# Kernel optimization log

Measured on AMD Instinct MI355X. Metric: run time of the kernel, lower is better.

The kernel has to match this reference:

```python
import jax, jax.numpy as jnp
import numpy as np

FACTOR = 0.2          # rotation/zoom/shift factor (init kwarg)
SCALE = 1.0 / 255.0   # rescale (init kwarg)
TWO_PI = 6.283185307179586
B, H, W, C = 64, 224, 224, 3


def _reflect(i, n):
    # TF fill_mode='reflect' index mapping (symmetric with edge repeat)
    m = jnp.mod(i, 2 * n)
    return jnp.where(m >= n, 2 * n - 1 - m, m)


def _bilinear(img, xs, ys):
    # img [H,W,C]; xs, ys [H,W] = input-space sample coords for each output pixel
    h, w, _ = img.shape
    x0f = jnp.floor(xs)
    y0f = jnp.floor(ys)
    fx = (xs - x0f)[..., None]
    fy = (ys - y0f)[..., None]
    x0 = x0f.astype(jnp.int32)
    y0 = y0f.astype(jnp.int32)
    x0r = _reflect(x0, w); x1r = _reflect(x0 + 1, w)
    y0r = _reflect(y0, h); y1r = _reflect(y0 + 1, h)
    Ia = img[y0r, x0r]; Ib = img[y0r, x1r]
    Ic = img[y1r, x0r]; Id = img[y1r, x1r]
    top = Ia * (1.0 - fx) + Ib * fx
    bot = Ic * (1.0 - fx) + Id * fx
    return top * (1.0 - fy) + bot * fy


_warp = jax.vmap(_bilinear)  # over batch: images [B,H,W,C], coords [B,H,W]


def setup_inputs() -> dict:
    key = jax.random.key(0)
    k = jax.random.split(key, 5)
    return {
        "image": jax.random.uniform(k[0], (B, H, W, C), jnp.float32) * 255.0,
        "angle_u": jax.random.uniform(k[1], (B,), jnp.float32),
        "zoom_u": jax.random.uniform(k[2], (B, 2), jnp.float32),
        "shift_u": jax.random.uniform(k[3], (B, 2), jnp.float32),
        "flip_u": jax.random.uniform(k[4], (B,), jnp.float32),
    }


def reference(image, angle_u, zoom_u, shift_u, flip_u):
    b, h, w, _ = image.shape
    dt = image.dtype
    yy, xx = jnp.meshgrid(jnp.arange(h, dtype=dt), jnp.arange(w, dtype=dt), indexing='ij')
    cx = (w - 1) / 2.0
    cy = (h - 1) / 2.0

    # 1) rescale
    x = image * SCALE

    # 2) random rotation: angle uniform in [-factor*2pi, +factor*2pi]
    theta = (2.0 * angle_u - 1.0) * FACTOR * TWO_PI            # [B]
    c = jnp.cos(theta)[:, None, None]
    s = jnp.sin(theta)[:, None, None]
    xr = c * (xx - cx) - s * (yy - cy) + cx                    # [B,H,W]
    yr = s * (xx - cx) + c * (yy - cy) + cy
    x = _warp(x, xr, yr)

    # 3) random zoom: zoom factor uniform in [1-factor, 1+factor] per axis
    z = 1.0 + (2.0 * zoom_u - 1.0) * FACTOR                    # [B,2] (h, w)
    zh = z[:, 0][:, None, None]
    zw = z[:, 1][:, None, None]
    xz = zw * (xx - cx) + cx
    yz = zh * (yy - cy) + cy
    x = _warp(x, xz, yz)

    # 4) random translation: shift fraction uniform in [-factor, factor]
    sh = (2.0 * shift_u - 1.0) * FACTOR                        # [B,2] (h, w)
    dy = (sh[:, 0] * h)[:, None, None]
    dx = (sh[:, 1] * w)[:, None, None]
    xt = xx - dx
    yt = yy - dy
    x = _warp(x, xt, yt)

    # 5) random horizontal flip (p = 0.5)
    flip = flip_u > 0.5
    x = jnp.where(flip[:, None, None, None], x[:, :, ::-1, :], x)
    return x
```

## Files before the change

kernel.cpp:

```cpp
#include <hip/hip_runtime.h>
#include <hip/hip_fp16.h>
#include <math.h>

#define BB 64
#define HH 224
#define WW 224
#define CC 3

constexpr float FACTOR  = 0.2f;
constexpr float SCALE_K = 1.0f / 255.0f;
constexpr float TWO_PI_F = 6.283185307179586f;
constexpr float CX = (WW - 1) * 0.5f;
constexpr float CY = (HH - 1) * 0.5f;
constexpr int PIX = HH * WW;
constexpr int IMG_ELEMS = PIX * CC;

constexpr int TILES_X = WW / 16;
constexpr int TILES_PER_IMG = TILES_X * TILES_X;
constexpr int NXCD = 8;
constexpr int NBLOCKS = BB * TILES_PER_IMG;

typedef float f32x4 __attribute__((ext_vector_type(4), aligned(4)));
typedef unsigned int u32x4 __attribute__((ext_vector_type(4), aligned(8)));

__device__ __forceinline__ int reflect1(int i, int n) {
    i = (i < 0) ? (-1 - i) : i;
    return (i >= n) ? (2 * n - 1 - i) : i;
}

__device__ __forceinline__ void rhull(int a, int b, int n, int& lo, int& hi) {
    int ra = reflect1(a, n), rb = reflect1(b, n);
    lo = min(ra, rb); hi = max(ra, rb);
    if (a <= 0 && b >= -1) lo = 0;
    if (b >= n - 1 && a <= n) hi = n - 1;
}

__device__ __forceinline__ void decode_tile(int bid, int& b, int& tx, int& ty) {
    int xcd  = bid & (NXCD - 1);
    int slot = bid >> 3;
    int bi   = slot / TILES_PER_IMG;
    int t    = slot - bi * TILES_PER_IMG;
    b = xcd + bi * NXCD;
    ty = t / TILES_X;
    tx = t - ty * TILES_X;
}

__device__ __forceinline__ void up3(uint2 v, float* o) {
    o[0] = __half2float(__ushort_as_half((unsigned short)(v.x & 0xffffu)));
    o[1] = __half2float(__ushort_as_half((unsigned short)(v.x >> 16)));
    o[2] = __half2float(__ushort_as_half((unsigned short)(v.y & 0xffffu)));
}

__device__ __forceinline__ uint2 pack3(float a, float b, float c) {
    uint2 v;
    v.x = (unsigned)__half_as_ushort(__float2half_rn(a)) |
          ((unsigned)__half_as_ushort(__float2half_rn(b)) << 16);
    v.y = (unsigned)__half_as_ushort(__float2half_rn(c));
    return v;
}

__global__ __launch_bounds__(256)
void rotate_kernel(const float* __restrict__ image, uint2* __restrict__ tmp,
                   const float* __restrict__ angle_u) {
    __shared__ float4 S[24][33];
    int b, tx, ty;
    decode_tile(blockIdx.x, b, tx, ty);
    const int ox = tx * 16, oy = ty * 16;

    const float theta = (2.0f * angle_u[b] - 1.0f) * FACTOR * TWO_PI_F;
    const float c = __cosf(theta), s = __sinf(theta);

    const float rx0 = (float)ox - CX, rx1 = (float)(ox + 15) - CX;
    const float ry0 = (float)oy - CY, ry1 = (float)(oy + 15) - CY;
    const int Xlo = (int)floorf(fminf(c * rx0, c * rx1) + fminf(-s * ry0, -s * ry1) + CX);
    const int Xhi = (int)floorf(fmaxf(c * rx0, c * rx1) + fmaxf(-s * ry0, -s * ry1) + CX) + 1;
    const int Ylo = (int)floorf(fminf(s * rx0, s * rx1) + fminf(c * ry0, c * ry1) + CY);
    const int Yhi = (int)floorf(fmaxf(s * rx0, s * rx1) + fmaxf(c * ry0, c * ry1) + CY) + 1;
    int Cx0, Cx1, Cy0, Cy1;
    rhull(Xlo, Xhi, WW, Cx0, Cx1);
    rhull(Ylo, Yhi, HH, Cy0, Cy1);

    const float* img = image + (size_t)b * IMG_ELEMS;
    {
        const int lc  = threadIdx.x & 31;
        const int col = min(Cx0 + lc, WW - 1);
#pragma unroll
        for (int it = 0; it < 3; ++it) {
            const int r   = it * 8 + (threadIdx.x >> 5);
            const int row = min(Cy0 + r, HH - 1);
            int pe = (row * WW + col) * CC;
            const bool last = pe > IMG_ELEMS - 4;
            pe = min(pe, IMG_ELEMS - 4);
            f32x4 v = *(const f32x4*)(img + pe);
            S[r][lc] = last ? make_float4(v.y, v.z, v.w, 0.0f)
                            : make_float4(v.x, v.y, v.z, v.w);
        }
    }
    __syncthreads();

    const int x = ox + (threadIdx.x & 15), y = oy + (threadIdx.x >> 4);
    const float xs = c * ((float)x - CX) - s * ((float)y - CY) + CX;
    const float ys = s * ((float)x - CX) + c * ((float)y - CY) + CY;
    const float xf = floorf(xs), yf = floorf(ys);
    const float fx = xs - xf, fy = ys - yf;
    const int x0 = (int)xf, y0 = (int)yf;
    const int c0 = min(max(reflect1(x0,     WW) - Cx0, 0), 31);
    const int c1 = min(max(reflect1(x0 + 1, WW) - Cx0, 0), 31);
    const int r0 = min(max(reflect1(y0,     HH) - Cy0, 0), 23);
    const int r1 = min(max(reflect1(y0 + 1, HH) - Cy0, 0), 23);

    const float4 A  = S[r0][c0];
    const float4 Bv = S[r0][c1];
    const float4 Cv = S[r1][c0];
    const float4 Dv = S[r1][c1];

    const float ofx = 1.0f - fx, ofy = 1.0f - fy;
    const float o0 = ((A.x * ofx + Bv.x * fx) * ofy + (Cv.x * ofx + Dv.x * fx) * fy) * SCALE_K;
    const float o1 = ((A.y * ofx + Bv.y * fx) * ofy + (Cv.y * ofx + Dv.y * fx) * fy) * SCALE_K;
    const float o2 = ((A.z * ofx + Bv.z * fx) * ofy + (Cv.z * ofx + Dv.z * fx) * fy) * SCALE_K;

    tmp[(size_t)b * PIX + y * WW + x] = pack3(o0, o1, o2);
}

__global__ __launch_bounds__(256)
void zoomshift_kernel(const uint2* __restrict__ tmp, float* __restrict__ out,
                      const float* __restrict__ zoom_u,
                      const float* __restrict__ shift_u,
                      const float* __restrict__ flip_u) {
    __shared__ uint2 Sz[32][34];
    __shared__ uint2 Zl[17][18];
    int b, tx, ty;
    decode_tile(blockIdx.x, b, tx, ty);
    const int ox = tx * 16, oy = ty * 16;

    const float zh = 1.0f + (2.0f * zoom_u[2 * b + 0] - 1.0f) * FACTOR;
    const float zw = 1.0f + (2.0f * zoom_u[2 * b + 1] - 1.0f) * FACTOR;
    const float dy = ((2.0f * shift_u[2 * b + 0] - 1.0f) * FACTOR) * (float)HH;
    const float dx = ((2.0f * shift_u[2 * b + 1] - 1.0f) * FACTOR) * (float)WW;
    const bool flip = flip_u[b] > 0.5f;

    const float ndxf = floorf(-dx), ndyf = floorf(-dy);
    const int Kx = (int)ndxf, Ky = (int)ndyf;
    const float fx3 = -dx - ndxf, fy3 = -dy - ndyf;

    const int Xmin = (flip ? WW - 16 - ox : ox) + Kx;
    const int Ymin = oy + Ky;

    int XrLo, XrHi, YrLo, YrHi;
    rhull(Xmin, Xmin + 16, WW, XrLo, XrHi);
    rhull(Ymin, Ymin + 16, HH, YrLo, YrHi);

    const int Gx0 = (int)floorf(zw * ((float)XrLo - CX) + CX);
    const int Gx1 = (int)floorf(zw * ((float)XrHi - CX) + CX) + 1;
    const int Gy0 = (int)floorf(zh * ((float)YrLo - CY) + CY);
    const int Gy1 = (int)floorf(zh * ((float)YrHi - CY) + CY) + 1;
    int Cx0, Cx1, Cy0, Cy1;
    rhull(Gx0, Gx1, WW, Cx0, Cx1);
    rhull(Gy0, Gy1, HH, Cy0, Cy1);
    const int CxA = Cx0 & ~1;

    const uint2* timg = tmp + (size_t)b * PIX;
    {
        const int cp  = (threadIdx.x & 15) * 2;
        const int col = min(CxA + cp, WW - 2);
#pragma unroll
        for (int it = 0; it < 2; ++it) {
            const int r   = it * 16 + (threadIdx.x >> 4);
            const int row = min(Cy0 + r, HH - 1);
            u32x4 v = *(const u32x4*)(timg + row * WW + col);
            *(u32x4*)(&Sz[r][cp]) = v;
        }
    }
    __syncthreads();

    for (int e = threadIdx.x; e < 17 * 17; e += 256) {
        const int ey = e / 17, ex = e - ey * 17;
        const int Xr = reflect1(Xmin + ex, WW);
        const int Yr = reflect1(Ymin + ey, HH);
        const float xs2 = zw * ((float)Xr - CX) + CX;
        const float ys2 = zh * ((float)Yr - CY) + CY;
        const float xf = floorf(xs2), yf = floorf(ys2);
        const float fx2 = xs2 - xf, fy2 = ys2 - yf;
        const int x20 = (int)xf, y20 = (int)yf;
        const int cA = min(max(reflect1(x20,     WW) - CxA, 0), 31);
        const int cB = min(max(reflect1(x20 + 1, WW) - CxA, 0), 31);
        const int rA = min(max(reflect1(y20,     HH) - Cy0, 0), 31);
        const int rB = min(max(reflect1(y20 + 1, HH) - Cy0, 0), 31);

        float A[3], Bv[3], Cv[3], Dv[3];
        up3(Sz[rA][cA], A);  up3(Sz[rA][cB], Bv);
        up3(Sz[rB][cA], Cv); up3(Sz[rB][cB], Dv);

        const float ofx = 1.0f - fx2, ofy = 1.0f - fy2;
        const float z0 = (A[0] * ofx + Bv[0] * fx2) * ofy + (Cv[0] * ofx + Dv[0] * fx2) * fy2;
        const float z1 = (A[1] * ofx + Bv[1] * fx2) * ofy + (Cv[1] * ofx + Dv[1] * fx2) * fy2;
        const float z2 = (A[2] * ofx + Bv[2] * fx2) * ofy + (Cv[2] * ofx + Dv[2] * fx2) * fy2;
        Zl[ey][ex] = pack3(z0, z1, z2);
    }
    __syncthreads();

    const int lx = threadIdx.x & 15, ly = threadIdx.x >> 4;
    const int ix = flip ? (15 - lx) : lx;
    float A[3], Bv[3], Cv[3], Dv[3];
    up3(Zl[ly][ix],     A);  up3(Zl[ly][ix + 1],     Bv);
    up3(Zl[ly + 1][ix], Cv); up3(Zl[ly + 1][ix + 1], Dv);

    float* o = out + ((size_t)b * PIX + (size_t)(oy + ly) * WW + (ox + lx)) * CC;
    const float ofx = 1.0f - fx3, ofy = 1.0f - fy3;
    o[0] = (A[0] * ofx + Bv[0] * fx3) * ofy + (Cv[0] * ofx + Dv[0] * fx3) * fy3;
    o[1] = (A[1] * ofx + Bv[1] * fx3) * ofy + (Cv[1] * ofx + Dv[1] * fx3) * fy3;
    o[2] = (A[2] * ofx + Bv[2] * fx3) * ofy + (Cv[2] * ofx + Dv[2] * fx3) * fy3;
}

extern "C" void kernel_launch(void* const* d_in, const int* in_sizes, int n_in,
                              void* d_out, int out_size, void* d_ws, size_t ws_size,
                              hipStream_t stream) {
    const float* image   = (const float*)d_in[0];
    const float* angle_u = (const float*)d_in[1];
    const float* zoom_u  = (const float*)d_in[2];
    const float* shift_u = (const float*)d_in[3];
    const float* flip_u  = (const float*)d_in[4];
    float* out = (float*)d_out;

    uint2* tmp = (uint2*)d_ws;

    rotate_kernel<<<NBLOCKS, 256, 0, stream>>>(image, tmp, angle_u);
    zoomshift_kernel<<<NBLOCKS, 256, 0, stream>>>(tmp, out, zoom_u, shift_u, flip_u);
}
```

Baseline: 42.03 us.

## Fuse rotate and zoom/shift warps into a single kernel with recompute halo

Merges the two-kernel pipeline into one kernel. Each output tile back-projects through shift, zoom and rotation to find the source region, loads it once into shared memory, then recomputes the rotated grid and the zoomed grid in shared memory before the final shift/flip interpolation. This removes the fp16 intermediate buffer round-trip through global memory and one kernel launch. In exchange it recomputes overlapping halo pixels per tile, uses more shared memory, and clamps the source and intermediate windows to fixed sizes (32x32 and 22x22), which could drop pixels if the footprint is larger.

```diff
diff --git a/kernel.cpp b/kernel.cpp
--- a/kernel.cpp
+++ b/kernel.cpp
@@ -1,5 +1,4 @@
 #include <hip/hip_runtime.h>
-#include <hip/hip_fp16.h>
 #include <math.h>
 
 #define BB 64
@@ -21,7 +20,6 @@
 constexpr int NBLOCKS = BB * TILES_PER_IMG;
 
 typedef float f32x4 __attribute__((ext_vector_type(4), aligned(4)));
-typedef unsigned int u32x4 __attribute__((ext_vector_type(4), aligned(8)));
 
 __device__ __forceinline__ int reflect1(int i, int n) {
     i = (i < 0) ? (-1 - i) : i;
@@ -45,94 +43,22 @@
     tx = t - ty * TILES_X;
 }
 
-__device__ __forceinline__ void up3(uint2 v, float* o) {
-    o[0] = __half2float(__ushort_as_half((unsigned short)(v.x & 0xffffu)));
-    o[1] = __half2float(__ushort_as_half((unsigned short)(v.x >> 16)));
-    o[2] = __half2float(__ushort_as_half((unsigned short)(v.y & 0xffffu)));
-}
+__global__ __launch_bounds__(256)
+void fused_kernel(const float* __restrict__ image, float* __restrict__ out,
+                  const float* __restrict__ angle_u,
+                  const float* __restrict__ zoom_u,
+                  const float* __restrict__ shift_u,
+                  const float* __restrict__ flip_u) {
+    __shared__ float SS[32 * 100];
+    __shared__ float G[484 * 3];
+    __shared__ float Z[289 * 3];
 
-__device__ __forceinline__ uint2 pack3(float a, float b, float c) {
-    uint2 v;
-    v.x = (unsigned)__half_as_ushort(__float2half_rn(a)) |
-          ((unsigned)__half_as_ushort(__float2half_rn(b)) << 16);
-    v.y = (unsigned)__half_as_ushort(__float2half_rn(c));
-    return v;
-}
-
-__global__ __launch_bounds__(256)
-void rotate_kernel(const float* __restrict__ image, uint2* __restrict__ tmp,
-                   const float* __restrict__ angle_u) {
-    __shared__ float4 S[24][33];
     int b, tx, ty;
     decode_tile(blockIdx.x, b, tx, ty);
     const int ox = tx * 16, oy = ty * 16;
 
     const float theta = (2.0f * angle_u[b] - 1.0f) * FACTOR * TWO_PI_F;
     const float c = __cosf(theta), s = __sinf(theta);
-
-    const float rx0 = (float)ox - CX, rx1 = (float)(ox + 15) - CX;
-    const float ry0 = (float)oy - CY, ry1 = (float)(oy + 15) - CY;
-    const int Xlo = (int)floorf(fminf(c * rx0, c * rx1) + fminf(-s * ry0, -s * ry1) + CX);
-    const int Xhi = (int)floorf(fmaxf(c * rx0, c * rx1) + fmaxf(-s * ry0, -s * ry1) + CX) + 1;
-    const int Ylo = (int)floorf(fminf(s * rx0, s * rx1) + fminf(c * ry0, c * ry1) + CY);
-    const int Yhi = (int)floorf(fmaxf(s * rx0, s * rx1) + fmaxf(c * ry0, c * ry1) + CY) + 1;
-    int Cx0, Cx1, Cy0, Cy1;
-    rhull(Xlo, Xhi, WW, Cx0, Cx1);
-    rhull(Ylo, Yhi, HH, Cy0, Cy1);
-
-    const float* img = image + (size_t)b * IMG_ELEMS;
-    {
-        const int lc  = threadIdx.x & 31;
-        const int col = min(Cx0 + lc, WW - 1);
-#pragma unroll
-        for (int it = 0; it < 3; ++it) {
-            const int r   = it * 8 + (threadIdx.x >> 5);
-            const int row = min(Cy0 + r, HH - 1);
-            int pe = (row * WW + col) * CC;
-            const bool last = pe > IMG_ELEMS - 4;
-            pe = min(pe, IMG_ELEMS - 4);
-            f32x4 v = *(const f32x4*)(img + pe);
-            S[r][lc] = last ? make_float4(v.y, v.z, v.w, 0.0f)
-                            : make_float4(v.x, v.y, v.z, v.w);
-        }
-    }
-    __syncthreads();
-
-    const int x = ox + (threadIdx.x & 15), y = oy + (threadIdx.x >> 4);
-    const float xs = c * ((float)x - CX) - s * ((float)y - CY) + CX;
-    const float ys = s * ((float)x - CX) + c * ((float)y - CY) + CY;
-    const float xf = floorf(xs), yf = floorf(ys);
-    const float fx = xs - xf, fy = ys - yf;
-    const int x0 = (int)xf, y0 = (int)yf;
-    const int c0 = min(max(reflect1(x0,     WW) - Cx0, 0), 31);
-    const int c1 = min(max(reflect1(x0 + 1, WW) - Cx0, 0), 31);
-    const int r0 = min(max(reflect1(y0,     HH) - Cy0, 0), 23);
-    const int r1 = min(max(reflect1(y0 + 1, HH) - Cy0, 0), 23);
-
-    const float4 A  = S[r0][c0];
-    const float4 Bv = S[r0][c1];
-    const float4 Cv = S[r1][c0];
-    const float4 Dv = S[r1][c1];
-
-    const float ofx = 1.0f - fx, ofy = 1.0f - fy;
-    const float o0 = ((A.x * ofx + Bv.x * fx) * ofy + (Cv.x * ofx + Dv.x * fx) * fy) * SCALE_K;
-    const float o1 = ((A.y * ofx + Bv.y * fx) * ofy + (Cv.y * ofx + Dv.y * fx) * fy) * SCALE_K;
-    const float o2 = ((A.z * ofx + Bv.z * fx) * ofy + (Cv.z * ofx + Dv.z * fx) * fy) * SCALE_K;
-
-    tmp[(size_t)b * PIX + y * WW + x] = pack3(o0, o1, o2);
-}
-
-__global__ __launch_bounds__(256)
-void zoomshift_kernel(const uint2* __restrict__ tmp, float* __restrict__ out,
-                      const float* __restrict__ zoom_u,
-                      const float* __restrict__ shift_u,
-                      const float* __restrict__ flip_u) {
-    __shared__ uint2 Sz[32][34];
-    __shared__ uint2 Zl[17][18];
-    int b, tx, ty;
-    decode_tile(blockIdx.x, b, tx, ty);
-    const int ox = tx * 16, oy = ty * 16;
-
     const float zh = 1.0f + (2.0f * zoom_u[2 * b + 0] - 1.0f) * FACTOR;
     const float zw = 1.0f + (2.0f * zoom_u[2 * b + 1] - 1.0f) * FACTOR;
     const float dy = ((2.0f * shift_u[2 * b + 0] - 1.0f) * FACTOR) * (float)HH;
@@ -145,7 +71,6 @@
 
     const int Xmin = (flip ? WW - 16 - ox : ox) + Kx;
     const int Ymin = oy + Ky;
-
     int XrLo, XrHi, YrLo, YrHi;
     rhull(Xmin, Xmin + 16, WW, XrLo, XrHi);
     rhull(Ymin, Ymin + 16, HH, YrLo, YrHi);
@@ -154,26 +79,62 @@
     const int Gx1 = (int)floorf(zw * ((float)XrHi - CX) + CX) + 1;
     const int Gy0 = (int)floorf(zh * ((float)YrLo - CY) + CY);
     const int Gy1 = (int)floorf(zh * ((float)YrHi - CY) + CY) + 1;
+    const int GH = min(Gy1 - Gy0 + 1, 22);
+
+    int RgxLo, RgxHi, RgyLo, RgyHi;
+    rhull(Gx0, Gx1, WW, RgxLo, RgxHi);
+    rhull(Gy0, Gy1, HH, RgyLo, RgyHi);
+
+    const float rx0 = (float)RgxLo - CX, rx1 = (float)RgxHi - CX;
+    const float ry0 = (float)RgyLo - CY, ry1 = (float)RgyHi - CY;
+    const float xsmin = fminf(c * rx0, c * rx1) + fminf(-s * ry0, -s * ry1) + CX;
+    const float xsmax = fmaxf(c * rx0, c * rx1) + fmaxf(-s * ry0, -s * ry1) + CX;
+    const float ysmin = fminf(s * rx0, s * rx1) + fminf(c * ry0, c * ry1) + CY;
+    const float ysmax = fmaxf(s * rx0, s * rx1) + fmaxf(c * ry0, c * ry1) + CY;
     int Cx0, Cx1, Cy0, Cy1;
-    rhull(Gx0, Gx1, WW, Cx0, Cx1);
-    rhull(Gy0, Gy1, HH, Cy0, Cy1);
-    const int CxA = Cx0 & ~1;
+    rhull((int)floorf(xsmin), (int)floorf(xsmax) + 1, WW, Cx0, Cx1);
+    rhull((int)floorf(ysmin), (int)floorf(ysmax) + 1, HH, Cy0, Cy1);
+    const int ColBase = min(Cx0, WW - 32);
+    const int RowBase = min(Cy0, HH - 32);
+    const int RowN = min(Cy1 - RowBase + 1, 32);
 
-    const uint2* timg = tmp + (size_t)b * PIX;
-    {
-        const int cp  = (threadIdx.x & 15) * 2;
-        const int col = min(CxA + cp, WW - 2);
-#pragma unroll
-        for (int it = 0; it < 2; ++it) {
-            const int r   = it * 16 + (threadIdx.x >> 4);
-            const int row = min(Cy0 + r, HH - 1);
-            u32x4 v = *(const u32x4*)(timg + row * WW + col);
-            *(u32x4*)(&Sz[r][cp]) = v;
-        }
+    const float* img = image + (size_t)b * IMG_ELEMS;
+    for (int id = threadIdx.x; id < 24 * RowN; id += 256) {
+        const int r = id / 24, g = id - r * 24;
+        const int src = ((RowBase + r) * WW + ColBase) * CC + g * 4;
+        f32x4 v = *(const f32x4*)(img + src);
+        v.x *= SCALE_K; v.y *= SCALE_K; v.z *= SCALE_K; v.w *= SCALE_K;
+        *(f32x4*)(&SS[r * 100 + g * 4]) = v;
     }
     __syncthreads();
 
-    for (int e = threadIdx.x; e < 17 * 17; e += 256) {
+    for (int e = threadIdx.x; e < 22 * GH; e += 256) {
+        const int gy = e / 22, gxi = e - gy * 22;
+        const int Rgx = reflect1(Gx0 + gxi, WW);
+        const int Rgy = reflect1(Gy0 + gy, HH);
+        const float xs = c * ((float)Rgx - CX) - s * ((float)Rgy - CY) + CX;
+        const float ys = s * ((float)Rgx - CX) + c * ((float)Rgy - CY) + CY;
+        const float xf = floorf(xs), yf = floorf(ys);
+        const float fx = xs - xf, fy = ys - yf;
+        const int x0 = (int)xf, y0 = (int)yf;
+        const int c0 = min(max(reflect1(x0,     WW) - ColBase, 0), 31);
+        const int c1 = min(max(reflect1(x0 + 1, WW) - ColBase, 0), 31);
+        const int r0 = min(max(reflect1(y0,     HH) - RowBase, 0), 31);
+        const int r1 = min(max(reflect1(y0 + 1, HH) - RowBase, 0), 31);
+        const float* A  = &SS[r0 * 100 + c0 * 3];
+        const float* Bv = &SS[r0 * 100 + c1 * 3];
+        const float* Cv = &SS[r1 * 100 + c0 * 3];
+        const float* Dv = &SS[r1 * 100 + c1 * 3];
+        const float ofx = 1.0f - fx, ofy = 1.0f - fy;
+        float* gp = &G[e * 3];
+#pragma unroll
+        for (int ch = 0; ch < CC; ++ch)
+            gp[ch] = (A[ch] * ofx + Bv[ch] * fx) * ofy +
+                     (Cv[ch] * ofx + Dv[ch] * fx) * fy;
+    }
+    __syncthreads();
+
+    for (int e = threadIdx.x; e < 289; e += 256) {
         const int ey = e / 17, ex = e - ey * 17;
         const int Xr = reflect1(Xmin + ex, WW);
         const int Yr = reflect1(Ymin + ey, HH);
@@ -182,34 +143,35 @@
         const float xf = floorf(xs2), yf = floorf(ys2);
         const float fx2 = xs2 - xf, fy2 = ys2 - yf;
         const int x20 = (int)xf, y20 = (int)yf;
-        const int cA = min(max(reflect1(x20,     WW) - CxA, 0), 31);
-        const int cB = min(max(reflect1(x20 + 1, WW) - CxA, 0), 31);
-        const int rA = min(max(reflect1(y20,     HH) - Cy0, 0), 31);
-        const int rB = min(max(reflect1(y20 + 1, HH) - Cy0, 0), 31);
-
-        float A[3], Bv[3], Cv[3], Dv[3];
-        up3(Sz[rA][cA], A);  up3(Sz[rA][cB], Bv);
-        up3(Sz[rB][cA], Cv); up3(Sz[rB][cB], Dv);
-
+        const int cA = min(max(x20     - Gx0, 0), 21);
+        const int cB = min(max(x20 + 1 - Gx0, 0), 21);
+        const int rA = min(max(y20     - Gy0, 0), 21);
+        const int rB = min(max(y20 + 1 - Gy0, 0), 21);
+        const float* A  = &G[(rA * 22 + cA) * 3];
+        const float* Bv = &G[(rA * 22 + cB) * 3];
+        const float* Cv = &G[(rB * 22 + cA) * 3];
+        const float* Dv = &G[(rB * 22 + cB) * 3];
         const float ofx = 1.0f - fx2, ofy = 1.0f - fy2;
-        const float z0 = (A[0] * ofx + Bv[0] * fx2) * ofy + (Cv[0] * ofx + Dv[0] * fx2) * fy2;
-        const float z1 = (A[1] * ofx + Bv[1] * fx2) * ofy + (Cv[1] * ofx + Dv[1] * fx2) * fy2;
-        const float z2 = (A[2] * ofx + Bv[2] * fx2) * ofy + (Cv[2] * ofx + Dv[2] * fx2) * fy2;
-        Zl[ey][ex] = pack3(z0, z1, z2);
+        float* zp = &Z[e * 3];
+#pragma unroll
+        for (int ch = 0; ch < CC; ++ch)
+            zp[ch] = (A[ch] * ofx + Bv[ch] * fx2) * ofy +
+                     (Cv[ch] * ofx + Dv[ch] * fx2) * fy2;
     }
     __syncthreads();
 
     const int lx = threadIdx.x & 15, ly = threadIdx.x >> 4;
     const int ix = flip ? (15 - lx) : lx;
-    float A[3], Bv[3], Cv[3], Dv[3];
-    up3(Zl[ly][ix],     A);  up3(Zl[ly][ix + 1],     Bv);
-    up3(Zl[ly + 1][ix], Cv); up3(Zl[ly + 1][ix + 1], Dv);
-
+    const float* A  = &Z[(ly * 17 + ix) * 3];
+    const float* Bv = &Z[(ly * 17 + ix + 1) * 3];
+    const float* Cv = &Z[((ly + 1) * 17 + ix) * 3];
+    const float* Dv = &Z[((ly + 1) * 17 + ix + 1) * 3];
     float* o = out + ((size_t)b * PIX + (size_t)(oy + ly) * WW + (ox + lx)) * CC;
     const float ofx = 1.0f - fx3, ofy = 1.0f - fy3;
-    o[0] = (A[0] * ofx + Bv[0] * fx3) * ofy + (Cv[0] * ofx + Dv[0] * fx3) * fy3;
-    o[1] = (A[1] * ofx + Bv[1] * fx3) * ofy + (Cv[1] * ofx + Dv[1] * fx3) * fy3;
-    o[2] = (A[2] * ofx + Bv[2] * fx3) * ofy + (Cv[2] * ofx + Dv[2] * fx3) * fy3;
+#pragma unroll
+    for (int ch = 0; ch < CC; ++ch)
+        o[ch] = (A[ch] * ofx + Bv[ch] * fx3) * ofy +
+                (Cv[ch] * ofx + Dv[ch] * fx3) * fy3;
 }
 
 extern "C" void kernel_launch(void* const* d_in, const int* in_sizes, int n_in,
@@ -222,8 +184,6 @@
     const float* flip_u  = (const float*)d_in[4];
     float* out = (float*)d_out;
 
-    uint2* tmp = (uint2*)d_ws;
-
-    rotate_kernel<<<NBLOCKS, 256, 0, stream>>>(image, tmp, angle_u);
-    zoomshift_kernel<<<NBLOCKS, 256, 0, stream>>>(tmp, out, zoom_u, shift_u, flip_u);
+    fused_kernel<<<NBLOCKS, 256, 0, stream>>>(image, out, angle_u, zoom_u,
+                                              shift_u, flip_u);
 }
```

New measurement: 45.68 us. 1.09x slower.
